# Performance work log

Measured on AMD Instinct MI355X. Metric: run time of the kernel, lower is better.

Reference implementation:

```python
import jax, jax.numpy as jnp
import numpy as np

B, T, D, H, W = 2, 16, 32, 64, 64
C2 = 2 * D          # channels after real/imag concat
E4 = 4 * C2         # para_pool expand=4
EPS = 1e-5


def _cnorm(z, g, b):
    # complex 'norm': LayerNorm over concat([real, imag], -1), then recombine
    zc = jnp.concatenate([z.real, z.imag], axis=-1)
    mu = zc.mean(-1, keepdims=True)
    var = zc.var(-1, keepdims=True)
    zn = (zc - mu) / jnp.sqrt(var + EPS) * g + b
    r, i = jnp.split(zn, 2, axis=-1)
    return r + 1j * i


def setup_inputs() -> dict:
    key = jax.random.key(0)
    ks = jax.random.split(key, 16)
    f = jnp.float32
    sd = 1.0 / np.sqrt(D)
    return {
        "x_real": jax.random.normal(ks[0], (B, T, D, H, W), f),
        "x_imag": jax.random.normal(ks[1], (B, T, D, H, W), f),
        "dt": jnp.ones((1,), f),
        "ln_s_g": jnp.ones((C2,), f), "ln_s_b": jnp.zeros((C2,), f),
        "conv_w": jax.random.normal(ks[2], (3, 3, C2, C2), f) * 0.05,
        "conv_b": jnp.zeros((C2,), f),
        "spec_fr": jax.random.normal(ks[3], (H, W, D), f) * 0.1,
        "spec_fi": jax.random.normal(ks[4], (H, W, D), f) * 0.1,
        "lam_r": -jnp.abs(jax.random.normal(ks[5], (D,), f)) * 0.5,
        "lam_i": jax.random.normal(ks[6], (D,), f),
        "E_r": jax.random.normal(ks[7], (D, D), f) * sd,
        "E_i": jax.random.normal(ks[8], (D, D), f) * sd,
        "Dm_r": jax.random.normal(ks[9], (D, D), f) * sd,
        "Dm_i": jax.random.normal(ks[10], (D, D), f) * sd,
        "ln_t_g": jnp.ones((C2,), f), "ln_t_b": jnp.zeros((C2,), f),
        "pool_w1": jax.random.normal(ks[11], (E4, C2), f) * 0.05,
        "pool_b1": jnp.zeros((E4,), f),
        "pool_w2": jax.random.normal(ks[12], (C2, E4), f) * 0.05,
        "pool_b2": jnp.zeros((C2,), f),
        "gate": jnp.full((1,), 0.5, f),
    }


def reference(x_real, x_imag, dt, ln_s_g, ln_s_b, conv_w, conv_b, spec_fr, spec_fi,
              lam_r, lam_i, E_r, E_i, Dm_r, Dm_i, ln_t_g, ln_t_b,
              pool_w1, pool_b1, pool_w2, pool_b2, gate):
    # work in channel-last layout [B,T,H,W,D]
    x = (x_real + 1j * x_imag).transpose(0, 1, 3, 4, 2)

    # ---- spatial block ----
    resid = x
    zn = _cnorm(x, ln_s_g, ln_s_b)                       # [B,T,H,W,D] complex
    zc = jnp.concatenate([zn.real, zn.imag], -1).reshape(B * T, H, W, C2)
    oc = jax.lax.conv_general_dilated(
        zc, conv_w, (1, 1), 'SAME',
        dimension_numbers=('NHWC', 'HWIO', 'NHWC')) + conv_b
    r, i = jnp.split(oc.reshape(B, T, H, W, C2), 2, axis=-1)
    cliff = r + 1j * i
    filt = spec_fr + 1j * spec_fi                         # [H,W,D]
    spec = jnp.fft.ifft2(jnp.fft.fft2(zn, axes=(2, 3)) * filt, axes=(2, 3))
    g = gate[0]
    x = g * cliff + (1.0 - g) * spec + resid

    # ---- temporal block: eigen-encode -> linear-decay scan -> decode ----
    resid = x
    xt = _cnorm(x.transpose(0, 2, 3, 1, 4).reshape(B * H * W, T, D), ln_t_g, ln_t_b)
    lam = lam_r + 1j * lam_i
    dts = dt[0]
    op_decay = jnp.exp(lam * dts)                         # [D]
    op_forcing = (jnp.exp(lam * dts) - 1.0) / lam          # [D] (exact ZOH forcing)
    Em = E_r + 1j * E_i
    Dm = Dm_r + 1j * Dm_i
    x_eig = jnp.einsum('ntd,de->nte', xt, Em)
    u = x_eig * op_forcing                                # [BHW,T,D]
    a = jnp.broadcast_to(op_decay, u.shape).astype(u.dtype)

    def comb(c1, c2):
        a1, u1 = c1
        a2, u2 = c2
        return (a1 * a2, u1 * a2 + u2)

    h = jax.lax.associative_scan(comb, (a, u), axis=1)[1]  # h_t = a_t h_{t-1} + u_t
    xo = jnp.einsum('ntd,de->nte', h, Dm).real
    x_drift = xo.reshape(B, H, W, T, D).transpose(0, 3, 1, 2, 4)
    x = x_drift + resid

    # ---- para pool (pointwise channel MLP on concat(real, imag)) ----
    resid = x
    xp = jnp.concatenate([x.real, x.imag], -1)            # [B,T,H,W,2D]
    y = jax.nn.gelu(jnp.einsum('bthwc,ec->bthwe', xp, pool_w1) + pool_b1)
    y = jnp.einsum('bthwe,ce->bthwc', y, pool_w2) + pool_b2
    r, i = jnp.split(y, 2, axis=-1)
    x = (r + 1j * i) + resid

    return x.transpose(0, 1, 4, 2, 3)                     # [B,T,D,H,W] complex
```

## Files before the change

### kernel.cpp

```cpp
#include <hip/hip_runtime.h>
#include <cstddef>


#define EPS_ 1e-5f
#define PI_  3.14159265358979323846f
#define ND_  4194304ull

typedef __attribute__((ext_vector_type(8))) short bf16x8;
typedef __attribute__((ext_vector_type(4))) float f32x4;

__device__ __forceinline__ short f2bf(float f) {
  unsigned u = __float_as_uint(f);
  unsigned r = (u + 0x7fffu + ((u >> 16) & 1u)) >> 16;
  return (short)r;
}
__device__ __forceinline__ float bf2f(short h) {
  return __uint_as_float(((unsigned)(unsigned short)h) << 16);
}

__global__ __launch_bounds__(256) void k0_prepw(
    const float* __restrict__ wgt, unsigned short* __restrict__ wb) {
  int j = blockIdx.x * 256 + threadIdx.x;
  int kk = j >> 12;
  int rem = j & 4095;
  int oc = rem >> 6;
  int ic = rem & 63;
  wb[j] = (unsigned short)f2bf(wgt[((size_t)kk * 64 + ic) * 64 + oc]);
}

__global__ __launch_bounds__(256) void k8_pool_prepw(
    const float* __restrict__ pw1, const float* __restrict__ pw2,
    unsigned short* __restrict__ pwb1, unsigned short* __restrict__ pwb2) {
  int j = blockIdx.x * 256 + threadIdx.x;
  if (j < 16384) {
    pwb1[j] = (unsigned short)f2bf(pw1[j]);
  } else {
    int j2 = j - 16384;
    int ec = j2 >> 12;
    int rem = j2 & 4095;
    int oc = rem >> 6;
    int el = rem & 63;
    pwb2[j2] = (unsigned short)f2bf(pw2[(size_t)oc * 256 + ec * 64 + el]);
  }
}

__global__ __launch_bounds__(256) void k1_cnorm_spatial(
    const float* __restrict__ xr, const float* __restrict__ xi,
    const float* __restrict__ g, const float* __restrict__ b,
    float* __restrict__ znr, float* __restrict__ zni,
    unsigned short* __restrict__ znb) {
  int tok = blockIdx.x * 256 + threadIdx.x;
  int bt = tok >> 12;
  int hw = tok & 4095;
  const float* pr = xr + (size_t)bt * 131072 + hw;
  const float* pi = xi + (size_t)bt * 131072 + hw;
  float r[32], q[32];
  float s = 0.f;
#pragma unroll
  for (int d = 0; d < 32; d++) {
    r[d] = pr[(size_t)d * 4096];
    q[d] = pi[(size_t)d * 4096];
    s += r[d] + q[d];
  }
  float mu = s * 0.015625f;
  float v = 0.f;
#pragma unroll
  for (int d = 0; d < 32; d++) {
    float a = r[d] - mu, c = q[d] - mu;
    v += a * a + c * c;
  }
  float rstd = rsqrtf(v * 0.015625f + EPS_);
#pragma unroll
  for (int d = 0; d < 32; d++) {
    r[d] = (r[d] - mu) * rstd * g[d] + b[d];
    q[d] = (q[d] - mu) * rstd * g[32 + d] + b[32 + d];
  }
  float4* outr = (float4*)(znr + (size_t)tok * 32);
  float4* outi = (float4*)(zni + (size_t)tok * 32);
#pragma unroll
  for (int j = 0; j < 8; j++) {
    outr[j] = make_float4(r[4 * j], r[4 * j + 1], r[4 * j + 2], r[4 * j + 3]);
    outi[j] = make_float4(q[4 * j], q[4 * j + 1], q[4 * j + 2], q[4 * j + 3]);
  }
  short* zb = (short*)(znb + (size_t)tok * 64);
#pragma unroll
  for (int j = 0; j < 4; j++) {
    bf16x8 vr, vq;
#pragma unroll
    for (int k = 0; k < 8; k++) {
      vr[k] = f2bf(r[8 * j + k]);
      vq[k] = f2bf(q[8 * j + k]);
    }
    *(bf16x8*)(zb + 8 * j) = vr;
    *(bf16x8*)(zb + 32 + 8 * j) = vq;
  }
}

__global__ __launch_bounds__(256) void k2_conv(
    const unsigned short* __restrict__ znb, const unsigned short* __restrict__ wb,
    const float* __restrict__ bias,
    float* __restrict__ clr, float* __restrict__ cli) {
  __shared__ __align__(16) short sA[3 * 66 * 88];
  __shared__ __align__(16) short sW[2][64 * 72];
  int h = blockIdx.x, bt = blockIdx.y;
  for (int v = threadIdx.x; v < 1584; v += 256) {
    int c0 = (v & 7) * 8;
    int row = v >> 3;
    int wp = row % 66;
    int rr = row / 66;
    int hh = h + rr - 1;
    int w = wp - 1;
    bf16x8 val = {0, 0, 0, 0, 0, 0, 0, 0};
    if ((unsigned)hh < 64u && (unsigned)w < 64u) {
      int tok = (bt * 64 + hh) * 64 + w;
      val = *(const bf16x8*)(znb + (size_t)tok * 64 + c0);
    }
    *(bf16x8*)(&sA[(rr * 66 + wp) * 88 + c0]) = val;
  }
  for (int v = threadIdx.x; v < 512; v += 256) {
    int oc = v >> 3, ic0 = (v & 7) * 8;
    *(bf16x8*)(&sW[0][oc * 72 + ic0]) = *(const bf16x8*)(wb + v * 8);
  }
  int lane = threadIdx.x & 63;
  int wv = threadIdx.x >> 6;
  int m0 = wv * 16;
  int lr = lane & 15;
  int quad = lane >> 4;
  f32x4 acc[4];
#pragma unroll
  for (int nt = 0; nt < 4; nt++) {
    float bz = bias[nt * 16 + lr];
    acc[nt][0] = bz; acc[nt][1] = bz; acc[nt][2] = bz; acc[nt][3] = bz;
  }
  __syncthreads();
  for (int kk = 0; kk < 9; kk++) {
    int cur = kk & 1;
    if (kk < 8) {
      const unsigned short* src = wb + (size_t)(kk + 1) * 4096;
      for (int v = threadIdx.x; v < 512; v += 256) {
        int oc = v >> 3, ic0 = (v & 7) * 8;
        *(bf16x8*)(&sW[cur ^ 1][oc * 72 + ic0]) = *(const bf16x8*)(src + v * 8);
      }
    }
    int kh = kk / 3, kw = kk - kh * 3;
    const short* arow = &sA[((size_t)kh * 66 + (m0 + lr + kw)) * 88 + quad * 8];
#pragma unroll
    for (int ks = 0; ks < 2; ks++) {
      bf16x8 afrag = *(const bf16x8*)(arow + ks * 32);
#pragma unroll
      for (int nt = 0; nt < 4; nt++) {
        bf16x8 bfrag = *(const bf16x8*)&sW[cur][(size_t)(nt * 16 + lr) * 72 + ks * 32 + quad * 8];
        acc[nt] = __builtin_amdgcn_mfma_f32_16x16x32_bf16(afrag, bfrag, acc[nt], 0, 0, 0);
      }
    }
    __syncthreads();
  }
  int tokbase = (bt * 64 + h) * 64 + m0;
#pragma unroll
  for (int nt = 0; nt < 4; nt++) {
    int oc = nt * 16 + lr;
    float* dst = (oc < 32) ? (clr + oc) : (cli + (oc - 32));
#pragma unroll
    for (int reg = 0; reg < 4; reg++) {
      int m = quad * 4 + reg;
      dst[(size_t)(tokbase + m) * 32] = acc[nt][reg];
    }
  }
}

__global__ __launch_bounds__(256) void k3_dftw(
    const float* __restrict__ znr, const float* __restrict__ zni,
    float* __restrict__ fqr, float* __restrict__ fqi) {
  __shared__ __align__(16) short sXh[64 * 72];
  __shared__ __align__(16) short sXl[64 * 72];
  __shared__ float twr[64], twi[64];
  int h = blockIdx.x, bt = blockIdx.y;
  size_t base = (size_t)((bt * 64 + h) * 64) * 32;
  if (threadIdx.x < 64) {
    float ang = -2.f * PI_ * (float)threadIdx.x * (1.f / 64.f);
    twr[threadIdx.x] = cosf(ang);
    twi[threadIdx.x] = sinf(ang);
  }
  for (int i = threadIdx.x; i < 2048; i += 256) {
    int w = i >> 5, d = i & 31;
    float vr = znr[base + i], vi = zni[base + i];
    short rh = f2bf(vr), ih = f2bf(vi);
    sXh[d * 72 + w] = rh;
    sXl[d * 72 + w] = f2bf(vr - bf2f(rh));
    sXh[(d + 32) * 72 + w] = ih;
    sXl[(d + 32) * 72 + w] = f2bf(vi - bf2f(ih));
  }
  __syncthreads();
  int lane = threadIdx.x & 63;
  int wv = threadIdx.x >> 6;
  int m0 = wv * 16;
  int lr = lane & 15;
  int quad = lane >> 4;
  int r = m0 + lr;
  bf16x8 tr0, tr1, ti0, ti1;
#pragma unroll
  for (int j = 0; j < 8; j++) {
    int i0 = (r * (quad * 8 + j)) & 63;
    int i1 = (r * (quad * 8 + j + 32)) & 63;
    tr0[j] = f2bf(twr[i0]); ti0[j] = f2bf(twi[i0]);
    tr1[j] = f2bf(twr[i1]); ti1[j] = f2bf(twi[i1]);
  }
  f32x4 p1[4], p2[4];
#pragma unroll
  for (int nt = 0; nt < 4; nt++) {
    p1[nt][0] = 0.f; p1[nt][1] = 0.f; p1[nt][2] = 0.f; p1[nt][3] = 0.f;
    p2[nt][0] = 0.f; p2[nt][1] = 0.f; p2[nt][2] = 0.f; p2[nt][3] = 0.f;
  }
#pragma unroll
  for (int ks = 0; ks < 2; ks++) {
    bf16x8 tr = ks ? tr1 : tr0;
    bf16x8 ti = ks ? ti1 : ti0;
#pragma unroll
    for (int nt = 0; nt < 4; nt++) {
      bf16x8 xh = *(const bf16x8*)&sXh[(size_t)(nt * 16 + lr) * 72 + ks * 32 + quad * 8];
      bf16x8 xl = *(const bf16x8*)&sXl[(size_t)(nt * 16 + lr) * 72 + ks * 32 + quad * 8];
      p1[nt] = __builtin_amdgcn_mfma_f32_16x16x32_bf16(tr, xh, p1[nt], 0, 0, 0);
      p1[nt] = __builtin_amdgcn_mfma_f32_16x16x32_bf16(tr, xl, p1[nt], 0, 0, 0);
      p2[nt] = __builtin_amdgcn_mfma_f32_16x16x32_bf16(ti, xh, p2[nt], 0, 0, 0);
      p2[nt] = __builtin_amdgcn_mfma_f32_16x16x32_bf16(ti, xl, p2[nt], 0, 0, 0);
    }
  }
#pragma unroll
  for (int nt = 0; nt < 2; nt++) {
#pragma unroll
    for (int reg = 0; reg < 4; reg++) {
      int k = m0 + quad * 4 + reg;
      int d = nt * 16 + lr;
      float Or = p1[nt][reg] - p2[nt + 2][reg];
      float Oi = p1[nt + 2][reg] + p2[nt][reg];
      size_t la = base + (size_t)k * 32 + d;
      fqr[la] = Or;
      fqi[la] = Oi;
    }
  }
}

__global__ __launch_bounds__(256) void k4_dfth(
    float* __restrict__ fqr, float* __restrict__ fqi,
    const float* __restrict__ flr, const float* __restrict__ fli) {
  __shared__ __align__(16) short sXh[64 * 72];
  __shared__ __align__(16) short sXl[64 * 72];
  __shared__ float twr[64], twi[64];
  int kw = blockIdx.x, bt = blockIdx.y;
  if (threadIdx.x < 64) {
    float ang = -2.f * PI_ * (float)threadIdx.x * (1.f / 64.f);
    twr[threadIdx.x] = cosf(ang);
    twi[threadIdx.x] = sinf(ang);
  }
  for (int i = threadIdx.x; i < 2048; i += 256) {
    int hh = i >> 5, d = i & 31;
    size_t ga = (size_t)((bt * 64 + hh) * 64 + kw) * 32 + d;
    float vr = fqr[ga], vi = fqi[ga];
    short rh = f2bf(vr), ih = f2bf(vi);
    sXh[d * 72 + hh] = rh;
    sXl[d * 72 + hh] = f2bf(vr - bf2f(rh));
    sXh[(d + 32) * 72 + hh] = ih;
    sXl[(d + 32) * 72 + hh] = f2bf(vi - bf2f(ih));
  }
  __syncthreads();
  int lane = threadIdx.x & 63;
  int wv = threadIdx.x >> 6;
  int m0 = wv * 16;
  int lr = lane & 15;
  int quad = lane >> 4;
  int r = m0 + lr;
  bf16x8 tr0, tr1, ti0, ti1;
#pragma unroll
  for (int j = 0; j < 8; j++) {
    int i0 = (r * (quad * 8 + j)) & 63;
    int i1 = (r * (quad * 8 + j + 32)) & 63;
    tr0[j] = f2bf(twr[i0]); ti0[j] = f2bf(twi[i0]);
    tr1[j] = f2bf(twr[i1]); ti1[j] = f2bf(twi[i1]);
  }
  f32x4 p1[4], p2[4];
#pragma unroll
  for (int nt = 0; nt < 4; nt++) {
    p1[nt][0] = 0.f; p1[nt][1] = 0.f; p1[nt][2] = 0.f; p1[nt][3] = 0.f;
    p2[nt][0] = 0.f; p2[nt][1] = 0.f; p2[nt][2] = 0.f; p2[nt][3] = 0.f;
  }
#pragma unroll
  for (int ks = 0; ks < 2; ks++) {
    bf16x8 tr = ks ? tr1 : tr0;
    bf16x8 ti = ks ? ti1 : ti0;
#pragma unroll
    for (int nt = 0; nt < 4; nt++) {
      bf16x8 xh = *(const bf16x8*)&sXh[(size_t)(nt * 16 + lr) * 72 + ks * 32 + quad * 8];
      bf16x8 xl = *(const bf16x8*)&sXl[(size_t)(nt * 16 + lr) * 72 + ks * 32 + quad * 8];
      p1[nt] = __builtin_amdgcn_mfma_f32_16x16x32_bf16(tr, xh, p1[nt], 0, 0, 0);
      p1[nt] = __builtin_amdgcn_mfma_f32_16x16x32_bf16(tr, xl, p1[nt], 0, 0, 0);
      p2[nt] = __builtin_amdgcn_mfma_f32_16x16x32_bf16(ti, xh, p2[nt], 0, 0, 0);
      p2[nt] = __builtin_amdgcn_mfma_f32_16x16x32_bf16(ti, xl, p2[nt], 0, 0, 0);
    }
  }
  __syncthreads();
#pragma unroll
  for (int nt = 0; nt < 2; nt++) {
#pragma unroll
    for (int reg = 0; reg < 4; reg++) {
      int kh = m0 + quad * 4 + reg;
      int d = nt * 16 + lr;
      float Or = p1[nt][reg] - p2[nt + 2][reg];
      float Oi = p1[nt + 2][reg] + p2[nt][reg];
      size_t fa = (size_t)(kh * 64 + kw) * 32 + d;
      float fr = flr[fa], fi = fli[fa];
      float pr = Or * fr - Oi * fi;
      float pi = Or * fi + Oi * fr;
      short ph = f2bf(pr);
      sXh[d * 72 + kh] = ph;
      sXl[d * 72 + kh] = f2bf(pr - bf2f(ph));
      short qh = f2bf(pi);
      sXh[(d + 32) * 72 + kh] = qh;
      sXl[(d + 32) * 72 + kh] = f2bf(pi - bf2f(qh));
    }
  }
  __syncthreads();
#pragma unroll
  for (int nt = 0; nt < 4; nt++) {
    p1[nt][0] = 0.f; p1[nt][1] = 0.f; p1[nt][2] = 0.f; p1[nt][3] = 0.f;
    p2[nt][0] = 0.f; p2[nt][1] = 0.f; p2[nt][2] = 0.f; p2[nt][3] = 0.f;
  }
#pragma unroll
  for (int ks = 0; ks < 2; ks++) {
    bf16x8 tr = ks ? tr1 : tr0;
    bf16x8 ti = ks ? ti1 : ti0;
#pragma unroll
    for (int nt = 0; nt < 4; nt++) {
      bf16x8 xh = *(const bf16x8*)&sXh[(size_t)(nt * 16 + lr) * 72 + ks * 32 + quad * 8];
      bf16x8 xl = *(const bf16x8*)&sXl[(size_t)(nt * 16 + lr) * 72 + ks * 32 + quad * 8];
      p1[nt] = __builtin_amdgcn_mfma_f32_16x16x32_bf16(tr, xh, p1[nt], 0, 0, 0);
      p1[nt] = __builtin_amdgcn_mfma_f32_16x16x32_bf16(tr, xl, p1[nt], 0, 0, 0);
      p2[nt] = __builtin_amdgcn_mfma_f32_16x16x32_bf16(ti, xh, p2[nt], 0, 0, 0);
      p2[nt] = __builtin_amdgcn_mfma_f32_16x16x32_bf16(ti, xl, p2[nt], 0, 0, 0);
    }
  }
#pragma unroll
  for (int nt = 0; nt < 2; nt++) {
#pragma unroll
    for (int reg = 0; reg < 4; reg++) {
      int hh = m0 + quad * 4 + reg;
      int d = nt * 16 + lr;
      float Or = (p1[nt][reg] + p2[nt + 2][reg]) * 0.015625f;
      float Oi = (p1[nt + 2][reg] - p2[nt][reg]) * 0.015625f;
      size_t ga = (size_t)((bt * 64 + hh) * 64 + kw) * 32 + d;
      fqr[ga] = Or;
      fqi[ga] = Oi;
    }
  }
}

__global__ __launch_bounds__(256) void k5_idftw_combine(
    const float* __restrict__ fqr, const float* __restrict__ fqi,
    const float* __restrict__ clr, const float* __restrict__ cli,
    const float* __restrict__ xr_in, const float* __restrict__ xi_in,
    const float* __restrict__ gate,
    float* __restrict__ xr, float* __restrict__ xi) {
  __shared__ __align__(16) short sXh[64 * 72];
  __shared__ __align__(16) short sXl[64 * 72];
  __shared__ float twr[64], twi[64];
  int h = blockIdx.x, bt = blockIdx.y;
  size_t base = (size_t)((bt * 64 + h) * 64) * 32;
  if (threadIdx.x < 64) {
    float ang = -2.f * PI_ * (float)threadIdx.x * (1.f / 64.f);
    twr[threadIdx.x] = cosf(ang);
    twi[threadIdx.x] = sinf(ang);
  }
  for (int i = threadIdx.x; i < 2048; i += 256) {
    int kw = i >> 5, d = i & 31;
    float vr = fqr[base + i], vi = fqi[base + i];
    short rh = f2bf(vr), ih = f2bf(vi);
    sXh[d * 72 + kw] = rh;
    sXl[d * 72 + kw] = f2bf(vr - bf2f(rh));
    sXh[(d + 32) * 72 + kw] = ih;
    sXl[(d + 32) * 72 + kw] = f2bf(vi - bf2f(ih));
  }
  __syncthreads();
  int lane = threadIdx.x & 63;
  int wv = threadIdx.x >> 6;
  int m0 = wv * 16;
  int lr = lane & 15;
  int quad = lane >> 4;
  int r = m0 + lr;
  bf16x8 tr0, tr1, ti0, ti1;
#pragma unroll
  for (int j = 0; j < 8; j++) {
    int i0 = (r * (quad * 8 + j)) & 63;
    int i1 = (r * (quad * 8 + j + 32)) & 63;
    tr0[j] = f2bf(twr[i0]); ti0[j] = f2bf(twi[i0]);
    tr1[j] = f2bf(twr[i1]); ti1[j] = f2bf(twi[i1]);
  }
  f32x4 p1[4], p2[4];
#pragma unroll
  for (int nt = 0; nt < 4; nt++) {
    p1[nt][0] = 0.f; p1[nt][1] = 0.f; p1[nt][2] = 0.f; p1[nt][3] = 0.f;
    p2[nt][0] = 0.f; p2[nt][1] = 0.f; p2[nt][2] = 0.f; p2[nt][3] = 0.f;
  }
#pragma unroll
  for (int ks = 0; ks < 2; ks++) {
    bf16x8 tr = ks ? tr1 : tr0;
    bf16x8 ti = ks ? ti1 : ti0;
#pragma unroll
    for (int nt = 0; nt < 4; nt++) {
      bf16x8 xh = *(const bf16x8*)&sXh[(size_t)(nt * 16 + lr) * 72 + ks * 32 + quad * 8];
      bf16x8 xl = *(const bf16x8*)&sXl[(size_t)(nt * 16 + lr) * 72 + ks * 32 + quad * 8];
      p1[nt] = __builtin_amdgcn_mfma_f32_16x16x32_bf16(tr, xh, p1[nt], 0, 0, 0);
      p1[nt] = __builtin_amdgcn_mfma_f32_16x16x32_bf16(tr, xl, p1[nt], 0, 0, 0);
      p2[nt] = __builtin_amdgcn_mfma_f32_16x16x32_bf16(ti, xh, p2[nt], 0, 0, 0);
      p2[nt] = __builtin_amdgcn_mfma_f32_16x16x32_bf16(ti, xl, p2[nt], 0, 0, 0);
    }
  }
  float g = gate[0];
  float gi = 1.f - g;
#pragma unroll
  for (int nt = 0; nt < 2; nt++) {
#pragma unroll
    for (int reg = 0; reg < 4; reg++) {
      int w = m0 + quad * 4 + reg;
      int d = nt * 16 + lr;
      float Or = (p1[nt][reg] + p2[nt + 2][reg]) * 0.015625f;
      float Oi = (p1[nt + 2][reg] - p2[nt][reg]) * 0.015625f;
      size_t la = base + (size_t)w * 32 + d;
      size_t ga = (size_t)(bt * 32 + d) * 4096 + h * 64 + w;
      xr[la] = g * clr[la] + gi * Or + xr_in[ga];
      xi[la] = g * cli[la] + gi * Oi + xi_in[ga];
    }
  }
}

__global__ __launch_bounds__(256) void k6_temporal(
    float* __restrict__ xr, float* __restrict__ xi,
    const float* __restrict__ lamr, const float* __restrict__ lami,
    const float* __restrict__ Er, const float* __restrict__ Ei,
    const float* __restrict__ Dmr, const float* __restrict__ Dmi,
    const float* __restrict__ lg, const float* __restrict__ lb,
    const float* __restrict__ dtp) {
  __shared__ float sEr[1024], sEi[1024], sDr[1024], sDi[1024];
  __shared__ __align__(16) float sXr[32 * 132];
  __shared__ __align__(16) float sXi[32 * 132];
  int n0 = blockIdx.x * 8;
  for (int i = threadIdx.x; i < 1024; i += 256) {
    sEr[i] = Er[i];
    sEi[i] = Ei[i];
    sDr[i] = Dmr[i];
    sDi[i] = Dmi[i];
  }
  if (threadIdx.x < 128) {
    int sIc = threadIdx.x >> 4;
    int t = threadIdx.x & 15;
    int n = n0 + sIc;
    int bb = n >> 12;
    int hw = n & 4095;
    size_t tokb = ((size_t)(bb * 16 + t)) * 4096 + hw;
    const float4* pr = (const float4*)(xr + tokb * 32);
    const float4* pi = (const float4*)(xi + tokb * 32);
    float rv[32], iv[32];
    float s = 0.f;
#pragma unroll
    for (int j = 0; j < 8; j++) {
      float4 a = pr[j];
      float4 c = pi[j];
      rv[4 * j] = a.x; rv[4 * j + 1] = a.y; rv[4 * j + 2] = a.z; rv[4 * j + 3] = a.w;
      iv[4 * j] = c.x; iv[4 * j + 1] = c.y; iv[4 * j + 2] = c.z; iv[4 * j + 3] = c.w;
      s += a.x + a.y + a.z + a.w + c.x + c.y + c.z + c.w;
    }
    float mu = s * 0.015625f;
    float v = 0.f;
#pragma unroll
    for (int d = 0; d < 32; d++) {
      float a = rv[d] - mu, c = iv[d] - mu;
      v += a * a + c * c;
    }
    float rstd = rsqrtf(v * 0.015625f + EPS_);
    int col = threadIdx.x;
#pragma unroll
    for (int d = 0; d < 32; d++) {
      sXr[d * 132 + col] = (rv[d] - mu) * rstd * lg[d] + lb[d];
      sXi[d * 132 + col] = (iv[d] - mu) * rstd * lg[32 + d] + lb[32 + d];
    }
  }
  __syncthreads();
  int sI = threadIdx.x >> 5;
  int e = threadIdx.x & 31;
  int tok0 = sI * 16;
  float dts = dtp[0];
  float lr = lamr[e], li = lami[e];
  float ex = expf(lr * dts);
  float dcr = ex * cosf(li * dts);
  float dci = ex * sinf(li * dts);
  float nr = dcr - 1.f, ni = dci;
  float invden = 1.f / (lr * lr + li * li);
  float fr = (nr * lr + ni * li) * invden;
  float fi = (ni * lr - nr * li) * invden;
  float xer[16], xei[16];
#pragma unroll
  for (int t = 0; t < 16; t++) { xer[t] = 0.f; xei[t] = 0.f; }
  for (int d = 0; d < 32; d++) {
    float er_ = sEr[d * 32 + e], ei_ = sEi[d * 32 + e];
    const float4* rb = (const float4*)&sXr[d * 132 + tok0];
    const float4* ib = (const float4*)&sXi[d * 132 + tok0];
#pragma unroll
    for (int j = 0; j < 4; j++) {
      float4 a4 = rb[j], c4 = ib[j];
      float av[4] = {a4.x, a4.y, a4.z, a4.w};
      float cv[4] = {c4.x, c4.y, c4.z, c4.w};
#pragma unroll
      for (int k = 0; k < 4; k++) {
        int t = 4 * j + k;
        xer[t] += av[k] * er_ - cv[k] * ei_;
        xei[t] += av[k] * ei_ + cv[k] * er_;
      }
    }
  }
  float hr = 0.f, hi = 0.f;
#pragma unroll
  for (int t = 0; t < 16; t++) {
    float ur = xer[t] * fr - xei[t] * fi;
    float ui = xer[t] * fi + xei[t] * fr;
    float t1 = dcr * hr - dci * hi + ur;
    hi = dcr * hi + dci * hr + ui;
    hr = t1;
    sXr[e * 132 + tok0 + t] = hr;
    sXi[e * 132 + tok0 + t] = hi;
  }
  __syncthreads();
  float oacc[16];
#pragma unroll
  for (int t = 0; t < 16; t++) oacc[t] = 0.f;
  for (int d = 0; d < 32; d++) {
    float dr_ = sDr[d * 32 + e], di_ = sDi[d * 32 + e];
    const float4* rb = (const float4*)&sXr[d * 132 + tok0];
    const float4* ib = (const float4*)&sXi[d * 132 + tok0];
#pragma unroll
    for (int j = 0; j < 4; j++) {
      float4 a4 = rb[j], c4 = ib[j];
      float av[4] = {a4.x, a4.y, a4.z, a4.w};
      float cv[4] = {c4.x, c4.y, c4.z, c4.w};
#pragma unroll
      for (int k = 0; k < 4; k++) {
        int t = 4 * j + k;
        oacc[t] += av[k] * dr_ - cv[k] * di_;
      }
    }
  }
  int n = n0 + sI;
  int bb = n >> 12;
  int hw = n & 4095;
#pragma unroll
  for (int t = 0; t < 16; t++) {
    size_t tokb = ((size_t)(bb * 16 + t)) * 4096 + hw;
    xr[tokb * 32 + e] += oacc[t];
  }
}

__global__ __launch_bounds__(256) void k7_pool(
    const float* __restrict__ xr, const float* __restrict__ xi,
    const unsigned short* __restrict__ pwb1, const float* __restrict__ pb1,
    const unsigned short* __restrict__ pwb2, const float* __restrict__ pb2,
    float* __restrict__ out, long long out_n) {
  __shared__ __align__(16) short sXh[64 * 72];
  __shared__ __align__(16) short sXl[64 * 72];
  __shared__ __align__(16) short sH[64 * 72];
  __shared__ __align__(16) short sW1[64 * 72];
  __shared__ __align__(16) short sW2[64 * 72];
  int tok0 = blockIdx.x * 64;
  for (int i = threadIdx.x; i < 4096; i += 256) {
    int t = i >> 6, c = i & 63;
    float v = (c < 32) ? xr[(size_t)(tok0 + t) * 32 + c]
                       : xi[(size_t)(tok0 + t) * 32 + c - 32];
    short hb = f2bf(v);
    sXh[t * 72 + c] = hb;
    sXl[t * 72 + c] = f2bf(v - bf2f(hb));
  }
  int lane = threadIdx.x & 63;
  int wv = threadIdx.x >> 6;
  int lr = lane & 15;
  int quad = lane >> 4;
  int m0 = wv * 16;
  f32x4 acc2[4];
#pragma unroll
  for (int nt = 0; nt < 4; nt++) {
    float bz = pb2[nt * 16 + lr];
    acc2[nt][0] = bz; acc2[nt][1] = bz; acc2[nt][2] = bz; acc2[nt][3] = bz;
  }
  const short* arh = &sXh[(size_t)(m0 + lr) * 72 + quad * 8];
  const short* arl = &sXl[(size_t)(m0 + lr) * 72 + quad * 8];
  const short* hrow = &sH[(size_t)(m0 + lr) * 72 + quad * 8];
  for (int ec = 0; ec < 4; ec++) {
    __syncthreads();
    {
      const unsigned short* w1 = pwb1 + (size_t)ec * 4096;
      const unsigned short* w2 = pwb2 + (size_t)ec * 4096;
      for (int v = threadIdx.x; v < 512; v += 256) {
        int row = v >> 3, c0 = (v & 7) * 8;
        *(bf16x8*)(&sW1[row * 72 + c0]) = *(const bf16x8*)(w1 + v * 8);
        *(bf16x8*)(&sW2[row * 72 + c0]) = *(const bf16x8*)(w2 + v * 8);
      }
    }
    __syncthreads();
    f32x4 acc1[4];
#pragma unroll
    for (int nt = 0; nt < 4; nt++) {
      float bz = pb1[ec * 64 + nt * 16 + lr];
      acc1[nt][0] = bz; acc1[nt][1] = bz; acc1[nt][2] = bz; acc1[nt][3] = bz;
    }
#pragma unroll
    for (int ks = 0; ks < 2; ks++) {
      bf16x8 ah = *(const bf16x8*)(arh + ks * 32);
      bf16x8 al = *(const bf16x8*)(arl + ks * 32);
#pragma unroll
      for (int nt = 0; nt < 4; nt++) {
        bf16x8 bfrag = *(const bf16x8*)&sW1[(size_t)(nt * 16 + lr) * 72 + ks * 32 + quad * 8];
        acc1[nt] = __builtin_amdgcn_mfma_f32_16x16x32_bf16(ah, bfrag, acc1[nt], 0, 0, 0);
        acc1[nt] = __builtin_amdgcn_mfma_f32_16x16x32_bf16(al, bfrag, acc1[nt], 0, 0, 0);
      }
    }
#pragma unroll
    for (int nt = 0; nt < 4; nt++) {
#pragma unroll
      for (int reg = 0; reg < 4; reg++) {
        float x = acc1[nt][reg];
        float u2 = 1.5957691216f * (x + 0.044715f * x * x * x);
        float e2 = __expf(u2);
        float gl = x - x * __builtin_amdgcn_rcpf(e2 + 1.f);
        sH[(m0 + quad * 4 + reg) * 72 + nt * 16 + lr] = f2bf(gl);
      }
    }
#pragma unroll
    for (int ks = 0; ks < 2; ks++) {
      bf16x8 af = *(const bf16x8*)(hrow + ks * 32);
#pragma unroll
      for (int nt = 0; nt < 4; nt++) {
        bf16x8 bfrag = *(const bf16x8*)&sW2[(size_t)(nt * 16 + lr) * 72 + ks * 32 + quad * 8];
        acc2[nt] = __builtin_amdgcn_mfma_f32_16x16x32_bf16(af, bfrag, acc2[nt], 0, 0, 0);
      }
    }
  }
#pragma unroll
  for (int nt = 0; nt < 4; nt++) {
    int oc = nt * 16 + lr;
#pragma unroll
    for (int reg = 0; reg < 4; reg++) {
      int t = tok0 + m0 + quad * 4 + reg;
      float resid = (oc < 32) ? xr[(size_t)t * 32 + oc] : xi[(size_t)t * 32 + oc - 32];
      float val = acc2[nt][reg] + resid;
      int bt = t >> 12;
      int hw = t & 4095;
      int d = (oc < 32) ? oc : oc - 32;
      size_t cidx = (size_t)(bt * 32 + d) * 4096 + hw;
      long long pos = (long long)cidx + ((oc < 32) ? 0ll : (long long)ND_);
      if (pos < out_n) out[pos] = val;
    }
  }
}

extern "C" void kernel_launch(void* const* d_in, const int* in_sizes, int n_in,
                              void* d_out, int out_size, void* d_ws, size_t ws_size,
                              hipStream_t stream) {
  (void)in_sizes; (void)n_in;
  const float* xr_in = (const float*)d_in[0];
  const float* xi_in = (const float*)d_in[1];
  const float* dt = (const float*)d_in[2];
  const float* ln_s_g = (const float*)d_in[3];
  const float* ln_s_b = (const float*)d_in[4];
  const float* conv_w = (const float*)d_in[5];
  const float* conv_b = (const float*)d_in[6];
  const float* spec_fr = (const float*)d_in[7];
  const float* spec_fi = (const float*)d_in[8];
  const float* lam_r = (const float*)d_in[9];
  const float* lam_i = (const float*)d_in[10];
  const float* E_r = (const float*)d_in[11];
  const float* E_i = (const float*)d_in[12];
  const float* Dm_r = (const float*)d_in[13];
  const float* Dm_i = (const float*)d_in[14];
  const float* ln_t_g = (const float*)d_in[15];
  const float* ln_t_b = (const float*)d_in[16];
  const float* pw1 = (const float*)d_in[17];
  const float* pb1 = (const float*)d_in[18];
  const float* pw2 = (const float*)d_in[19];
  const float* pb2 = (const float*)d_in[20];
  const float* gate = (const float*)d_in[21];

  if (ws_size < 6ull * ND_ * 4ull) return;

  float* ws = (float*)d_ws;
  float* znr = ws;
  float* zni = ws + ND_;
  float* clr = ws + 2 * ND_;
  float* cli = ws + 3 * ND_;
  float* fqr = ws + 4 * ND_;
  float* fqi = ws + 5 * ND_;
  float* out = (float*)d_out;
  unsigned short* znb = (unsigned short*)fqr;
  unsigned short* wb = (unsigned short*)fqi;
  unsigned short* pwb1 = (unsigned short*)fqr;
  unsigned short* pwb2 = pwb1 + 16384;

  k0_prepw<<<144, 256, 0, stream>>>(conv_w, wb);
  k1_cnorm_spatial<<<512, 256, 0, stream>>>(xr_in, xi_in, ln_s_g, ln_s_b, znr, zni, znb);
  k2_conv<<<dim3(64, 32), 256, 0, stream>>>(znb, wb, conv_b, clr, cli);
  k3_dftw<<<dim3(64, 32), 256, 0, stream>>>(znr, zni, fqr, fqi);
  k4_dfth<<<dim3(64, 32), 256, 0, stream>>>(fqr, fqi, spec_fr, spec_fi);
  k5_idftw_combine<<<dim3(64, 32), 256, 0, stream>>>(fqr, fqi, clr, cli, xr_in, xi_in,
                                                     gate, znr, zni);
  k8_pool_prepw<<<128, 256, 0, stream>>>(pw1, pw2, pwb1, pwb2);
  k6_temporal<<<1024, 256, 0, stream>>>(znr, zni, lam_r, lam_i, E_r, E_i, Dm_r, Dm_i,
                                        ln_t_g, ln_t_b, dt);
  k7_pool<<<2048, 256, 0, stream>>>(znr, zni, pwb1, pb1, pwb2, pb2, out, (long long)out_size);
}
```

Measured before the change: 311.4 us.

## Move temporal block projections to bf16 MFMA with split-precision and warp-parallel scan

Rewrites the temporal kernel so the complex E and Dm projections run as bf16 MFMA matmuls. Activations are split into hi/lo bf16 pairs to keep near-fp32 accuracy, and the weights are pre-packed into bf16 by the existing prep kernel. The sequential 16-step recurrence becomes a per-lane 4-step local scan combined across quads with shuffles. The goal is to replace scalar FMA loops with matrix-core work, at the cost of bf16 weight rounding error and extra shared-memory traffic for the hi/lo copies.

```diff
diff --git a/kernel.cpp b/kernel.cpp
--- a/kernel.cpp
+++ b/kernel.cpp
@@ -30,17 +30,36 @@
 
 __global__ __launch_bounds__(256) void k8_pool_prepw(
     const float* __restrict__ pw1, const float* __restrict__ pw2,
-    unsigned short* __restrict__ pwb1, unsigned short* __restrict__ pwb2) {
+    const float* __restrict__ Er, const float* __restrict__ Ei,
+    const float* __restrict__ Dmr, const float* __restrict__ Dmi,
+    unsigned short* __restrict__ pwb1, unsigned short* __restrict__ pwb2,
+    unsigned short* __restrict__ eB, unsigned short* __restrict__ dB) {
   int j = blockIdx.x * 256 + threadIdx.x;
   if (j < 16384) {
     pwb1[j] = (unsigned short)f2bf(pw1[j]);
-  } else {
+  } else if (j < 32768) {
     int j2 = j - 16384;
     int ec = j2 >> 12;
     int rem = j2 & 4095;
     int oc = rem >> 6;
     int el = rem & 63;
     pwb2[j2] = (unsigned short)f2bf(pw2[(size_t)oc * 256 + ec * 64 + el]);
+  } else if (j < 36864) {
+    int j2 = j - 32768;
+    int col = j2 >> 6, k = j2 & 63;
+    float v;
+    if (col < 32) {
+      v = (k < 32) ? Er[k * 32 + col] : -Ei[(k - 32) * 32 + col];
+    } else {
+      int e = col - 32;
+      v = (k < 32) ? Ei[k * 32 + e] : Er[(k - 32) * 32 + e];
+    }
+    eB[j2] = (unsigned short)f2bf(v);
+  } else if (j < 38912) {
+    int j2 = j - 36864;
+    int e2 = j2 >> 6, k = j2 & 63;
+    float v = (k < 32) ? Dmr[k * 32 + e2] : -Dmi[(k - 32) * 32 + e2];
+    dB[j2] = (unsigned short)f2bf(v);
   }
 }
 
@@ -434,19 +453,22 @@
 __global__ __launch_bounds__(256) void k6_temporal(
     float* __restrict__ xr, float* __restrict__ xi,
     const float* __restrict__ lamr, const float* __restrict__ lami,
-    const float* __restrict__ Er, const float* __restrict__ Ei,
-    const float* __restrict__ Dmr, const float* __restrict__ Dmi,
+    const unsigned short* __restrict__ eB, const unsigned short* __restrict__ dB,
     const float* __restrict__ lg, const float* __restrict__ lb,
     const float* __restrict__ dtp) {
-  __shared__ float sEr[1024], sEi[1024], sDr[1024], sDi[1024];
-  __shared__ __align__(16) float sXr[32 * 132];
-  __shared__ __align__(16) float sXi[32 * 132];
+  __shared__ __align__(16) short sAh[128 * 72];
+  __shared__ __align__(16) short sAl[128 * 72];
+  __shared__ __align__(16) short sBe[64 * 72];
+  __shared__ __align__(16) short sBd[32 * 72];
   int n0 = blockIdx.x * 8;
-  for (int i = threadIdx.x; i < 1024; i += 256) {
-    sEr[i] = Er[i];
-    sEi[i] = Ei[i];
-    sDr[i] = Dmr[i];
-    sDi[i] = Dmi[i];
+  for (int v = threadIdx.x; v < 768; v += 256) {
+    int c0 = (v & 7) * 8;
+    if (v < 512) {
+      *(bf16x8*)(&sBe[(v >> 3) * 72 + c0]) = *(const bf16x8*)(eB + v * 8);
+    } else {
+      int v2 = v - 512;
+      *(bf16x8*)(&sBd[(v2 >> 3) * 72 + c0]) = *(const bf16x8*)(dB + v2 * 8);
+    }
   }
   if (threadIdx.x < 128) {
     int sIc = threadIdx.x >> 4;
@@ -475,84 +497,153 @@
       v += a * a + c * c;
     }
     float rstd = rsqrtf(v * 0.015625f + EPS_);
-    int col = threadIdx.x;
-#pragma unroll
-    for (int d = 0; d < 32; d++) {
-      sXr[d * 132 + col] = (rv[d] - mu) * rstd * lg[d] + lb[d];
-      sXi[d * 132 + col] = (iv[d] - mu) * rstd * lg[32 + d] + lb[32 + d];
+    int row = threadIdx.x * 72;
+#pragma unroll
+    for (int j = 0; j < 4; j++) {
+      bf16x8 vh, vl, wh, wl;
+#pragma unroll
+      for (int k = 0; k < 8; k++) {
+        float a = (rv[8 * j + k] - mu) * rstd * lg[8 * j + k] + lb[8 * j + k];
+        float c = (iv[8 * j + k] - mu) * rstd * lg[32 + 8 * j + k] + lb[32 + 8 * j + k];
+        short ah = f2bf(a);
+        vh[k] = ah; vl[k] = f2bf(a - bf2f(ah));
+        short ch = f2bf(c);
+        wh[k] = ch; wl[k] = f2bf(c - bf2f(ch));
+      }
+      *(bf16x8*)(&sAh[row + 8 * j]) = vh;
+      *(bf16x8*)(&sAl[row + 8 * j]) = vl;
+      *(bf16x8*)(&sAh[row + 32 + 8 * j]) = wh;
+      *(bf16x8*)(&sAl[row + 32 + 8 * j]) = wl;
     }
   }
   __syncthreads();
-  int sI = threadIdx.x >> 5;
-  int e = threadIdx.x & 31;
-  int tok0 = sI * 16;
+  int lane = threadIdx.x & 63;
+  int wv = threadIdx.x >> 6;
+  int lr = lane & 15;
+  int quad = lane >> 4;
+  f32x4 p[2][4];
+#pragma unroll
+  for (int m = 0; m < 2; m++)
+#pragma unroll
+    for (int nt = 0; nt < 4; nt++) {
+      p[m][nt][0] = 0.f; p[m][nt][1] = 0.f; p[m][nt][2] = 0.f; p[m][nt][3] = 0.f;
+    }
+#pragma unroll
+  for (int m = 0; m < 2; m++) {
+    int rowA = ((2 * wv + m) * 16 + lr) * 72;
+#pragma unroll
+    for (int ks = 0; ks < 2; ks++) {
+      bf16x8 ah = *(const bf16x8*)&sAh[rowA + ks * 32 + quad * 8];
+      bf16x8 al = *(const bf16x8*)&sAl[rowA + ks * 32 + quad * 8];
+#pragma unroll
+      for (int nt = 0; nt < 4; nt++) {
+        bf16x8 bfrag = *(const bf16x8*)&sBe[(nt * 16 + lr) * 72 + ks * 32 + quad * 8];
+        p[m][nt] = __builtin_amdgcn_mfma_f32_16x16x32_bf16(ah, bfrag, p[m][nt], 0, 0, 0);
+        p[m][nt] = __builtin_amdgcn_mfma_f32_16x16x32_bf16(al, bfrag, p[m][nt], 0, 0, 0);
+      }
+    }
+  }
   float dts = dtp[0];
-  float lr = lamr[e], li = lami[e];
-  float ex = expf(lr * dts);
-  float dcr = ex * cosf(li * dts);
-  float dci = ex * sinf(li * dts);
-  float nr = dcr - 1.f, ni = dci;
-  float invden = 1.f / (lr * lr + li * li);
-  float fr = (nr * lr + ni * li) * invden;
-  float fi = (ni * lr - nr * li) * invden;
-  float xer[16], xei[16];
-#pragma unroll
-  for (int t = 0; t < 16; t++) { xer[t] = 0.f; xei[t] = 0.f; }
-  for (int d = 0; d < 32; d++) {
-    float er_ = sEr[d * 32 + e], ei_ = sEi[d * 32 + e];
-    const float4* rb = (const float4*)&sXr[d * 132 + tok0];
-    const float4* ib = (const float4*)&sXi[d * 132 + tok0];
-#pragma unroll
-    for (int j = 0; j < 4; j++) {
-      float4 a4 = rb[j], c4 = ib[j];
-      float av[4] = {a4.x, a4.y, a4.z, a4.w};
-      float cv[4] = {c4.x, c4.y, c4.z, c4.w};
-#pragma unroll
-      for (int k = 0; k < 4; k++) {
-        int t = 4 * j + k;
-        xer[t] += av[k] * er_ - cv[k] * ei_;
-        xei[t] += av[k] * ei_ + cv[k] * er_;
-      }
-    }
-  }
-  float hr = 0.f, hi = 0.f;
-#pragma unroll
-  for (int t = 0; t < 16; t++) {
-    float ur = xer[t] * fr - xei[t] * fi;
-    float ui = xer[t] * fi + xei[t] * fr;
-    float t1 = dcr * hr - dci * hi + ur;
-    hi = dcr * hi + dci * hr + ui;
-    hr = t1;
-    sXr[e * 132 + tok0 + t] = hr;
-    sXi[e * 132 + tok0 + t] = hi;
+  float acr[2], aci[2], fcr[2], fci[2];
+#pragma unroll
+  for (int eo = 0; eo < 2; eo++) {
+    int e = eo * 16 + lr;
+    float lrr = lamr[e], lii = lami[e];
+    float ex = expf(lrr * dts);
+    float dcr = ex * cosf(lii * dts);
+    float dci = ex * sinf(lii * dts);
+    acr[eo] = dcr; aci[eo] = dci;
+    float nr = dcr - 1.f, ni = dci;
+    float invden = 1.f / (lrr * lrr + lii * lii);
+    fcr[eo] = (nr * lrr + ni * lii) * invden;
+    fci[eo] = (ni * lrr - nr * lii) * invden;
+  }
+#pragma unroll
+  for (int m = 0; m < 2; m++) {
+#pragma unroll
+    for (int eo = 0; eo < 2; eo++) {
+      float ar = acr[eo], ai_ = aci[eo];
+      float fr = fcr[eo], fi = fci[eo];
+      float a2r = ar * ar - ai_ * ai_, a2i = 2.f * ar * ai_;
+      float a3r = a2r * ar - a2i * ai_, a3i = a2r * ai_ + a2i * ar;
+      float a4r = a2r * a2r - a2i * a2i, a4i = 2.f * a2r * a2i;
+      float a8r = a4r * a4r - a4i * a4i, a8i = 2.f * a4r * a4i;
+      float apr[4] = {ar, a2r, a3r, a4r};
+      float api[4] = {ai_, a2i, a3i, a4i};
+      float hlr[4], hli[4];
+#pragma unroll
+      for (int reg = 0; reg < 4; reg++) {
+        float xr_ = p[m][eo][reg], xi_ = p[m][2 + eo][reg];
+        float ur = xr_ * fr - xi_ * fi;
+        float ui = xr_ * fi + xi_ * fr;
+        if (reg == 0) {
+          hlr[0] = ur; hli[0] = ui;
+        } else {
+          float t1 = ar * hlr[reg - 1] - ai_ * hli[reg - 1] + ur;
+          float t2 = ar * hli[reg - 1] + ai_ * hlr[reg - 1] + ui;
+          hlr[reg] = t1; hli[reg] = t2;
+        }
+      }
+      float Sr = hlr[3], Si = hli[3];
+      float t1r = __shfl_up(Sr, 16), t1i = __shfl_up(Si, 16);
+      if (quad >= 1) { Sr += a4r * t1r - a4i * t1i; Si += a4r * t1i + a4i * t1r; }
+      float t2r = __shfl_up(Sr, 32), t2i = __shfl_up(Si, 32);
+      if (quad >= 2) { Sr += a8r * t2r - a8i * t2i; Si += a8r * t2i + a8i * t2r; }
+      float hinr = __shfl_up(Sr, 16), hini = __shfl_up(Si, 16);
+      if (quad == 0) { hinr = 0.f; hini = 0.f; }
+      int e = eo * 16 + lr;
+#pragma unroll
+      for (int reg = 0; reg < 4; reg++) {
+        float hr_ = apr[reg] * hinr - api[reg] * hini + hlr[reg];
+        float hi_ = apr[reg] * hini + api[reg] * hinr + hli[reg];
+        int row = ((2 * wv + m) * 16 + quad * 4 + reg) * 72;
+        short b1 = f2bf(hr_);
+        sAh[row + e] = b1;
+        sAl[row + e] = f2bf(hr_ - bf2f(b1));
+        short b2 = f2bf(hi_);
+        sAh[row + 32 + e] = b2;
+        sAl[row + 32 + e] = f2bf(hi_ - bf2f(b2));
+      }
+    }
   }
   __syncthreads();
-  float oacc[16];
-#pragma unroll
-  for (int t = 0; t < 16; t++) oacc[t] = 0.f;
-  for (int d = 0; d < 32; d++) {
-    float dr_ = sDr[d * 32 + e], di_ = sDi[d * 32 + e];
-    const float4* rb = (const float4*)&sXr[d * 132 + tok0];
-    const float4* ib = (const float4*)&sXi[d * 132 + tok0];
-#pragma unroll
-    for (int j = 0; j < 4; j++) {
-      float4 a4 = rb[j], c4 = ib[j];
-      float av[4] = {a4.x, a4.y, a4.z, a4.w};
-      float cv[4] = {c4.x, c4.y, c4.z, c4.w};
-#pragma unroll
-      for (int k = 0; k < 4; k++) {
-        int t = 4 * j + k;
-        oacc[t] += av[k] * dr_ - cv[k] * di_;
-      }
-    }
-  }
-  int n = n0 + sI;
-  int bb = n >> 12;
-  int hw = n & 4095;
-#pragma unroll
-  for (int t = 0; t < 16; t++) {
-    size_t tokb = ((size_t)(bb * 16 + t)) * 4096 + hw;
-    xr[tokb * 32 + e] += oacc[t];
+  f32x4 q[2][2];
+#pragma unroll
+  for (int m = 0; m < 2; m++)
+#pragma unroll
+    for (int nt = 0; nt < 2; nt++) {
+      q[m][nt][0] = 0.f; q[m][nt][1] = 0.f; q[m][nt][2] = 0.f; q[m][nt][3] = 0.f;
+    }
+#pragma unroll
+  for (int m = 0; m < 2; m++) {
+    int rowA = ((2 * wv + m) * 16 + lr) * 72;
+#pragma unroll
+    for (int ks = 0; ks < 2; ks++) {
+      bf16x8 ah = *(const bf16x8*)&sAh[rowA + ks * 32 + quad * 8];
+      bf16x8 al = *(const bf16x8*)&sAl[rowA + ks * 32 + quad * 8];
+#pragma unroll
+      for (int nt = 0; nt < 2; nt++) {
+        bf16x8 bfrag = *(const bf16x8*)&sBd[(nt * 16 + lr) * 72 + ks * 32 + quad * 8];
+        q[m][nt] = __builtin_amdgcn_mfma_f32_16x16x32_bf16(ah, bfrag, q[m][nt], 0, 0, 0);
+        q[m][nt] = __builtin_amdgcn_mfma_f32_16x16x32_bf16(al, bfrag, q[m][nt], 0, 0, 0);
+      }
+    }
+  }
+#pragma unroll
+  for (int m = 0; m < 2; m++) {
+    int n = n0 + 2 * wv + m;
+    int bb = n >> 12;
+    int hw = n & 4095;
+#pragma unroll
+    for (int nt = 0; nt < 2; nt++) {
+      int e2 = nt * 16 + lr;
+#pragma unroll
+      for (int reg = 0; reg < 4; reg++) {
+        int t = quad * 4 + reg;
+        size_t tokb = ((size_t)(bb * 16 + t)) * 4096 + hw;
+        xr[tokb * 32 + e2] += q[m][nt][reg];
+      }
+    }
   }
 }
 
@@ -698,6 +789,8 @@
   unsigned short* wb = (unsigned short*)fqi;
   unsigned short* pwb1 = (unsigned short*)fqr;
   unsigned short* pwb2 = pwb1 + 16384;
+  unsigned short* eB = pwb1 + 32768;
+  unsigned short* dB = pwb1 + 36864;
 
   k0_prepw<<<144, 256, 0, stream>>>(conv_w, wb);
   k1_cnorm_spatial<<<512, 256, 0, stream>>>(xr_in, xi_in, ln_s_g, ln_s_b, znr, zni, znb);
@@ -706,8 +799,9 @@
   k4_dfth<<<dim3(64, 32), 256, 0, stream>>>(fqr, fqi, spec_fr, spec_fi);
   k5_idftw_combine<<<dim3(64, 32), 256, 0, stream>>>(fqr, fqi, clr, cli, xr_in, xi_in,
                                                      gate, znr, zni);
-  k8_pool_prepw<<<128, 256, 0, stream>>>(pw1, pw2, pwb1, pwb2);
-  k6_temporal<<<1024, 256, 0, stream>>>(znr, zni, lam_r, lam_i, E_r, E_i, Dm_r, Dm_i,
+  k8_pool_prepw<<<156, 256, 0, stream>>>(pw1, pw2, E_r, E_i, Dm_r, Dm_i,
+                                         pwb1, pwb2, eB, dB);
+  k6_temporal<<<1024, 256, 0, stream>>>(znr, zni, lam_r, lam_i, eB, dB,
                                         ln_t_g, ln_t_b, dt);
   k7_pool<<<2048, 256, 0, stream>>>(znr, zni, pwb1, pb1, pwb2, pb2, out, (long long)out_size);
 }
```

Result: faster. 299.3 us (-3.9%).
